# Optimization experiments

Hardware: AMD Instinct MI355X
Metric: run time of the kernel (lower is better)

## Reference

```python
import jax, jax.numpy as jnp
import numpy as np
import math

B, N, D = 16, 2048, 256

def setup_inputs() -> dict:
    key = jax.random.key(0)
    kq, kk, kv = jax.random.split(key, 3)
    query = jax.random.normal(kq, (B, N, D), dtype=jnp.float32)
    k = jax.random.normal(kk, (B, N, D), dtype=jnp.float32)
    value = jax.random.normal(kv, (B, D, N), dtype=jnp.float32)  # channel-first [B, d_v, N]
    return {"query": query, "key": k, "value": value, "mask": 0}

def reference(query, key, value, mask):
    d_k = query.shape[-1]
    scale = 1.0 / math.sqrt(d_k)
    # scores: [B, N, N]
    scores = jnp.einsum('bnd,bmd->bnm', query, key) * scale
    p_attn = jax.nn.softmax(scores, axis=-1)
    # mask is a static Python int flag gating dropout; mask=0 -> no dropout (deterministic reference)
    if mask:
        pass  # dropout intentionally disabled in deterministic reference
    # out = p_attn @ value^T  -> [B, N, d_v]; module returns out.transpose(-2,-1) -> [B, d_v, N]
    out_t = jnp.einsum('bnm,bdm->bdn', p_attn, value)
    return (out_t, p_attn)
```

## Files before the change

kernel.cpp:

```cpp
#include <hip/hip_runtime.h>
#include <hip/hip_bf16.h>


using bf16x8 = __attribute__((ext_vector_type(8))) short;
using f32x4  = __attribute__((ext_vector_type(4))) float;

__device__ __forceinline__ short f2bf(float f) {
    unsigned u = __float_as_uint(f);
    u += 0x7fffu + ((u >> 16) & 1u);
    return (short)(u >> 16);
}

__device__ __forceinline__ f32x4 mfma16(bf16x8 a, bf16x8 b, f32x4 c) {
    return __builtin_amdgcn_mfma_f32_16x16x32_bf16(a, b, c, 0, 0, 0);
}

#define AS1(p) ((const __attribute__((address_space(1))) void*)(p))
#define AS3(p) ((__attribute__((address_space(3))) void*)(p))

__global__ __launch_bounds__(256)
void convert_qkv(const float* __restrict__ Q, const float* __restrict__ K,
                 const float* __restrict__ V, short* __restrict__ Qb,
                 short* __restrict__ Kb, short* __restrict__ Vb, size_t n8)
{
    size_t i = (size_t)blockIdx.x * 256 + threadIdx.x;
    const float* src;
    short* dst;
    float scale = 1.0f;
    if (i < n8)            { src = Q;  dst = Qb; scale = 0.0625f; }
    else if (i < 2 * n8)   { i -= n8;      src = K; dst = Kb; }
    else                   { i -= 2 * n8;  src = V; dst = Vb; }
    const f32x4* s4 = (const f32x4*)src;
    f32x4 a = __builtin_nontemporal_load(s4 + i * 2);
    f32x4 b = __builtin_nontemporal_load(s4 + i * 2 + 1);
    bf16x8 v;
    v[0] = f2bf(a[0] * scale); v[1] = f2bf(a[1] * scale);
    v[2] = f2bf(a[2] * scale); v[3] = f2bf(a[3] * scale);
    v[4] = f2bf(b[0] * scale); v[5] = f2bf(b[1] * scale);
    v[6] = f2bf(b[2] * scale); v[7] = f2bf(b[3] * scale);
    *(bf16x8*)(dst + i * 8) = v;
}

__global__ __launch_bounds__(512, 2)
void fused_attn(const short* __restrict__ Qb, const short* __restrict__ Kb,
                const short* __restrict__ Vb, float* __restrict__ Pout,
                float* __restrict__ outT)
{
    __shared__ __align__(16) short Klds[2][64 * 256];
    __shared__ __align__(16) short Vlds[2][256 * 64];
    __shared__ __align__(16) short Plds[128 * 64];
    float* lpart = (float*)Plds;

    constexpr float LOG2E = 1.4426950408889634f;

    const unsigned g  = blockIdx.x;
    const unsigned wg = (g & 7) * 32 + (g >> 3);
    const int b  = (int)(wg >> 4);
    const int nb = (int)(wg & 15);

    const int tid  = threadIdx.x;
    const int lane = tid & 63;
    const int wave = tid >> 6;
    const int wn  = wave >> 1;
    const int wm  = wave & 1;
    const int l15 = lane & 15;
    const int l4  = lane >> 4;

    const short* Kbase = Kb + (size_t)b * (2048 * 256);
    const short* Vbase = Vb + (size_t)b * (256 * 2048);

    const short* Qp = Qb + ((size_t)b * 2048 + (size_t)nb * 128) * 256;
    bf16x8 qf[2][8];
#pragma unroll
    for (int mf = 0; mf < 2; mf++)
#pragma unroll
        for (int ks = 0; ks < 8; ks++)
            qf[mf][ks] = *(const bf16x8*)(
                Qp + (size_t)(wn * 32 + mf * 16 + l15) * 256 + ks * 32 + l4 * 8);

    auto stage_k = [&](int t, int buf) {
#pragma unroll
        for (int i = 0; i < 4; i++) {
            int ml = i * 16 + wave * 2 + (lane >> 5);
            int c  = lane & 31;
            int cs = (c & 24) | ((c ^ ml) & 7);
            __builtin_amdgcn_global_load_lds(
                AS1(Kbase + (size_t)(t * 64 + ml) * 256 + cs * 8),
                AS3(&Klds[buf][i * 4096 + wave * 512]), 16, 0, 0);
        }
    };
    auto stage_v = [&](int t, int buf) {
#pragma unroll
        for (int i = 0; i < 4; i++) {
            int d  = i * 64 + wave * 8 + (lane >> 3);
            int c  = lane & 7;
            int cs = c ^ (d & 7);
            __builtin_amdgcn_global_load_lds(
                AS1(Vbase + (size_t)d * 2048 + t * 64 + cs * 8),
                AS3(&Vlds[buf][i * 4096 + wave * 512]), 16, 0, 0);
        }
    };

    auto qkt = [&](int buf, f32x4 sacT[2][2]) {
#pragma unroll
        for (int ks = 0; ks < 8; ks++) {
            bf16x8 kf[2];
#pragma unroll
            for (int nf = 0; nf < 2; nf++) {
                int m  = wm * 32 + nf * 16 + l15;
                int ch = (ks * 4 + l4) ^ (m & 7);
                kf[nf] = *(const bf16x8*)((const char*)&Klds[buf][0] + m * 512 + ch * 16);
            }
#pragma unroll
            for (int mf = 0; mf < 2; mf++)
#pragma unroll
                for (int nf = 0; nf < 2; nf++)
                    sacT[mf][nf] = mfma16(kf[nf], qf[mf][ks], sacT[mf][nf]);
        }
    };

    float lacc[2] = {0.f, 0.f};
    stage_k(0, 0);
    for (int t = 0; t < 32; t++) {
        __syncthreads();
        if (t + 1 < 32) stage_k(t + 1, (t + 1) & 1);
        f32x4 sacT[2][2];
#pragma unroll
        for (int mf = 0; mf < 2; mf++)
#pragma unroll
            for (int nf = 0; nf < 2; nf++)
                sacT[mf][nf] = f32x4{0.f, 0.f, 0.f, 0.f};
        qkt(t & 1, sacT);
#pragma unroll
        for (int mf = 0; mf < 2; mf++)
#pragma unroll
            for (int nf = 0; nf < 2; nf++)
#pragma unroll
                for (int r = 0; r < 4; r++)
                    lacc[mf] += exp2f(sacT[mf][nf][r] * LOG2E);
    }
#pragma unroll
    for (int mf = 0; mf < 2; mf++) {
        lacc[mf] += __shfl_xor(lacc[mf], 16);
        lacc[mf] += __shfl_xor(lacc[mf], 32);
    }
    if (l4 == 0) {
        lpart[wave * 32 + 0 * 16 + l15] = lacc[0];
        lpart[wave * 32 + 1 * 16 + l15] = lacc[1];
    }
    __syncthreads();
    float rl[2];
#pragma unroll
    for (int mf = 0; mf < 2; mf++)
        rl[mf] = 1.0f / (lpart[(wn * 2 + 0) * 32 + mf * 16 + l15] +
                         lpart[(wn * 2 + 1) * 32 + mf * 16 + l15]);

    f32x4 oac[4][4];
#pragma unroll
    for (int i = 0; i < 4; i++)
#pragma unroll
        for (int j = 0; j < 4; j++)
            oac[i][j] = f32x4{0.f, 0.f, 0.f, 0.f};

    stage_k(0, 0);
    stage_v(0, 0);
    float* prow = Pout + ((size_t)b * 2048 + (size_t)nb * 128) * 2048;

    for (int t = 0; t < 32; t++) {
        __syncthreads();
        f32x4 sacT[2][2];
#pragma unroll
        for (int mf = 0; mf < 2; mf++)
#pragma unroll
            for (int nf = 0; nf < 2; nf++)
                sacT[mf][nf] = f32x4{0.f, 0.f, 0.f, 0.f};
        qkt(t & 1, sacT);

        f32x4 pv4[2][2];
#pragma unroll
        for (int mf = 0; mf < 2; mf++)
#pragma unroll
            for (int nf = 0; nf < 2; nf++) {
#pragma unroll
                for (int r = 0; r < 4; r++)
                    pv4[mf][nf][r] = exp2f(sacT[mf][nf][r] * LOG2E) * rl[mf];
                short4 ps;
                ps.x = f2bf(pv4[mf][nf][0]); ps.y = f2bf(pv4[mf][nf][1]);
                ps.z = f2bf(pv4[mf][nf][2]); ps.w = f2bf(pv4[mf][nf][3]);
                const int n  = wn * 32 + mf * 16 + l15;
                const int mb = wm * 32 + nf * 16 + l4 * 4;
                const int ch = (mb >> 3) ^ (n & 7);
                *(short4*)((char*)Plds + n * 128 + ch * 16 + (mb & 7) * 2) = ps;
            }
        __syncthreads();

        if (t + 1 < 32) {
            stage_k(t + 1, (t + 1) & 1);
            stage_v(t + 1, (t + 1) & 1);
        }

#pragma unroll
        for (int mf = 0; mf < 2; mf++)
#pragma unroll
            for (int nf = 0; nf < 2; nf++) {
                const int n  = wn * 32 + mf * 16 + l15;
                const int m  = t * 64 + wm * 32 + nf * 16 + l4 * 4;
                __builtin_nontemporal_store(pv4[mf][nf],
                    (f32x4*)(prow + (size_t)n * 2048 + m));
            }

        const char* vb_ = (const char*)&Vlds[t & 1][0];
#pragma unroll
        for (int ksl = 0; ksl < 2; ksl++) {
            bf16x8 vf[4], pf[4];
#pragma unroll
            for (int mf4 = 0; mf4 < 4; mf4++) {
                const int d  = wn * 64 + mf4 * 16 + l15;
                const int ch = (ksl * 4 + l4) ^ (d & 7);
                vf[mf4] = *(const bf16x8*)(vb_ + d * 128 + ch * 16);
            }
#pragma unroll
            for (int nf4 = 0; nf4 < 4; nf4++) {
                const int n  = wm * 64 + nf4 * 16 + l15;
                const int ch = (ksl * 4 + l4) ^ (n & 7);
                pf[nf4] = *(const bf16x8*)((const char*)Plds + n * 128 + ch * 16);
            }
#pragma unroll
            for (int mf4 = 0; mf4 < 4; mf4++)
#pragma unroll
                for (int nf4 = 0; nf4 < 4; nf4++)
                    oac[mf4][nf4] = mfma16(vf[mf4], pf[nf4], oac[mf4][nf4]);
        }
    }

    float* op = outT + (size_t)b * (256 * 2048) + (size_t)nb * 128;
#pragma unroll
    for (int mf4 = 0; mf4 < 4; mf4++)
#pragma unroll
        for (int nf4 = 0; nf4 < 4; nf4++)
#pragma unroll
            for (int r = 0; r < 4; r++) {
                int d = wn * 64 + mf4 * 16 + l4 * 4 + r;
                int n = wm * 64 + nf4 * 16 + l15;
                op[(size_t)d * 2048 + n] = oac[mf4][nf4][r];
            }
}

template<int BM, int BN, int BK>
__global__ __launch_bounds__(256)
void gemm_abt(const float* __restrict__ A, const float* __restrict__ B,
              float* __restrict__ C, int M, int N, int K,
              long strideA, long strideB, long strideC, float scale)
{
    const int b  = blockIdx.z;
    const int bm = blockIdx.y;
    const int bn = blockIdx.x;
    A += (size_t)b * strideA;
    B += (size_t)b * strideB;
    C += (size_t)b * strideC;

    constexpr int LDT = BK + 8;
    __shared__ __align__(16) short Alds[BM][LDT];
    __shared__ __align__(16) short Blds[BN][LDT];

    const int tid  = threadIdx.x;
    const int lane = tid & 63;
    const int wave = tid >> 6;
    const int wr   = wave >> 1;
    const int wc   = wave & 1;

    f32x4 acc[4][4];
#pragma unroll
    for (int m = 0; m < 4; m++)
#pragma unroll
        for (int n = 0; n < 4; n++)
            acc[m][n] = f32x4{0.f, 0.f, 0.f, 0.f};

    const float* Ab = A + (size_t)(bm * BM) * K;
    const float* Bb = B + (size_t)(bn * BN) * K;

    const int tr  = tid >> 4;
    const int tc4 = (tid & 15) << 2;

    for (int k0 = 0; k0 < K; k0 += BK) {
        __syncthreads();
#pragma unroll
        for (int r = tr; r < BM; r += 16) {
            const float4 v = *(const float4*)(Ab + (size_t)r * K + k0 + tc4);
            short4 s;
            s.x = f2bf(v.x); s.y = f2bf(v.y); s.z = f2bf(v.z); s.w = f2bf(v.w);
            *(short4*)&Alds[r][tc4] = s;
        }
#pragma unroll
        for (int r = tr; r < BN; r += 16) {
            const float4 v = *(const float4*)(Bb + (size_t)r * K + k0 + tc4);
            short4 s;
            s.x = f2bf(v.x); s.y = f2bf(v.y); s.z = f2bf(v.z); s.w = f2bf(v.w);
            *(short4*)&Blds[r][tc4] = s;
        }
        __syncthreads();

#pragma unroll
        for (int kk = 0; kk < BK; kk += 32) {
            const int ko = kk + ((lane >> 4) << 3);
            bf16x8 af[4], bfr[4];
#pragma unroll
            for (int m = 0; m < 4; m++)
                af[m] = *(const bf16x8*)&Alds[wr * 64 + m * 16 + (lane & 15)][ko];
#pragma unroll
            for (int n = 0; n < 4; n++)
                bfr[n] = *(const bf16x8*)&Blds[wc * 64 + n * 16 + (lane & 15)][ko];
#pragma unroll
            for (int m = 0; m < 4; m++)
#pragma unroll
                for (int n = 0; n < 4; n++)
                    acc[m][n] = __builtin_amdgcn_mfma_f32_16x16x32_bf16(
                        af[m], bfr[n], acc[m][n], 0, 0, 0);
        }
    }

    float* Cb = C + (size_t)(bm * BM) * N + (size_t)bn * BN;
    const int rbase = wr * 64 + ((lane >> 4) << 2);
    const int cbase = wc * 64 + (lane & 15);
#pragma unroll
    for (int m = 0; m < 4; m++)
#pragma unroll
        for (int n = 0; n < 4; n++)
#pragma unroll
            for (int r = 0; r < 4; r++)
                Cb[(size_t)(rbase + m * 16 + r) * N + cbase + n * 16] =
                    acc[m][n][r] * scale;
}

__global__ __launch_bounds__(256)
void softmax_rows(float* __restrict__ P)
{
    const size_t row = blockIdx.x;
    float* p = P + row * 2048;
    const int tid  = threadIdx.x;
    const int lane = tid & 63;
    const int wave = tid >> 6;

    float4 v0 = ((const float4*)p)[tid];
    float4 v1 = ((const float4*)p)[tid + 256];

    float m = fmaxf(fmaxf(fmaxf(v0.x, v0.y), fmaxf(v0.z, v0.w)),
                    fmaxf(fmaxf(v1.x, v1.y), fmaxf(v1.z, v1.w)));
#pragma unroll
    for (int off = 32; off; off >>= 1) m = fmaxf(m, __shfl_xor(m, off));

    __shared__ float sred[4];
    __shared__ float ssum[4];
    if (lane == 0) sred[wave] = m;
    __syncthreads();
    m = fmaxf(fmaxf(sred[0], sred[1]), fmaxf(sred[2], sred[3]));

    v0.x = expf(v0.x - m); v0.y = expf(v0.y - m);
    v0.z = expf(v0.z - m); v0.w = expf(v0.w - m);
    v1.x = expf(v1.x - m); v1.y = expf(v1.y - m);
    v1.z = expf(v1.z - m); v1.w = expf(v1.w - m);

    float s = (v0.x + v0.y + v0.z + v0.w) + (v1.x + v1.y + v1.z + v1.w);
#pragma unroll
    for (int off = 32; off; off >>= 1) s += __shfl_xor(s, off);
    if (lane == 0) ssum[wave] = s;
    __syncthreads();
    s = ssum[0] + ssum[1] + ssum[2] + ssum[3];

    const float r = 1.0f / s;
    v0.x *= r; v0.y *= r; v0.z *= r; v0.w *= r;
    v1.x *= r; v1.y *= r; v1.z *= r; v1.w *= r;

    ((float4*)p)[tid]       = v0;
    ((float4*)p)[tid + 256] = v1;
}

extern "C" void kernel_launch(void* const* d_in, const int* in_sizes, int n_in,
                              void* d_out, int out_size, void* d_ws, size_t ws_size,
                              hipStream_t stream)
{
    const float* Q  = (const float*)d_in[0];
    const float* Kk = (const float*)d_in[1];
    const float* V  = (const float*)d_in[2];

    float* outT = (float*)d_out;
    float* P    = outT + (size_t)16 * 256 * 2048;

    const size_t nQ = (size_t)16 * 2048 * 256;
    const long sQK = (long)2048 * 256;
    const long sP  = (long)2048 * 2048;
    const long sO  = (long)256 * 2048;

    const size_t needQKV = 3 * nQ * sizeof(short);

    if (ws_size >= needQKV) {
        short* Qb = (short*)d_ws;
        short* Kb = Qb + nQ;
        short* Vb = Kb + nQ;

        convert_qkv<<<dim3((unsigned)(3 * nQ / 8 / 256)), 256, 0, stream>>>(
            Q, Kk, V, Qb, Kb, Vb, nQ / 8);

        fused_attn<<<dim3(256), 512, 0, stream>>>(Qb, Kb, Vb, P, outT);
    } else {
        gemm_abt<128, 128, 64><<<dim3(16, 16, 16), 256, 0, stream>>>(
            Q, Kk, P, 2048, 2048, 256, sQK, sQK, sP, 0.0625f);
        softmax_rows<<<dim3(16 * 2048), 256, 0, stream>>>(P);
        gemm_abt<128, 128, 64><<<dim3(16, 2, 16), 256, 0, stream>>>(
            V, P, outT, 256, 2048, 2048, sO, sP, sO, 1.0f);
    }
}
```

Baseline: 185.1 us.

## Use 128-row K tiles in the row-sum pass and raise MFMA wave priority

The first (row-sum) pass now stages 128 K rows per step. It uses the whole K and V LDS arrays as its two buffers, which halves the loop trips and barriers for that pass. The prefetch of the first K and V tiles for the second pass is moved earlier, so it overlaps the row-sum reduction. s_setprio is raised around the MFMA sections so matrix work is favoured over the store and exp waves. The cost is more accumulator registers in the first pass, which could add register pressure at 2 blocks per CU.

```diff
diff --git a/kernel.cpp b/kernel.cpp
--- a/kernel.cpp
+++ b/kernel.cpp
@@ -10,13 +10,14 @@
     u += 0x7fffu + ((u >> 16) & 1u);
     return (short)(u >> 16);
 }
-
 __device__ __forceinline__ f32x4 mfma16(bf16x8 a, bf16x8 b, f32x4 c) {
     return __builtin_amdgcn_mfma_f32_16x16x32_bf16(a, b, c, 0, 0, 0);
 }
 
 #define AS1(p) ((const __attribute__((address_space(1))) void*)(p))
 #define AS3(p) ((__attribute__((address_space(3))) void*)(p))
+
+constexpr float LOG2E = 1.4426950408889634f;
 
 __global__ __launch_bounds__(256)
 void convert_qkv(const float* __restrict__ Q, const float* __restrict__ K,
@@ -51,8 +52,6 @@
     __shared__ __align__(16) short Plds[128 * 64];
     float* lpart = (float*)Plds;
 
-    constexpr float LOG2E = 1.4426950408889634f;
-
     const unsigned g  = blockIdx.x;
     const unsigned wg = (g & 7) * 32 + (g >> 3);
     const int b  = (int)(wg >> 4);
@@ -100,8 +99,21 @@
                 AS3(&Vlds[buf][i * 4096 + wave * 512]), 16, 0, 0);
         }
     };
+    auto stage_k128 = [&](int t, int which) {
+#pragma unroll
+        for (int i = 0; i < 8; i++) {
+            int ml = i * 16 + wave * 2 + (lane >> 5);
+            int c  = lane & 31;
+            int cs = (c & 24) | ((c ^ ml) & 7);
+            short* dst = which ? &Vlds[0][0] : &Klds[0][0];
+            __builtin_amdgcn_global_load_lds(
+                AS1(Kbase + (size_t)(t * 128 + ml) * 256 + cs * 8),
+                AS3(dst + i * 4096 + wave * 512), 16, 0, 0);
+        }
+    };
 
     auto qkt = [&](int buf, f32x4 sacT[2][2]) {
+        __builtin_amdgcn_s_setprio(1);
 #pragma unroll
         for (int ks = 0; ks < 8; ks++) {
             bf16x8 kf[2];
@@ -117,28 +129,50 @@
                 for (int nf = 0; nf < 2; nf++)
                     sacT[mf][nf] = mfma16(kf[nf], qf[mf][ks], sacT[mf][nf]);
         }
+        __builtin_amdgcn_s_setprio(0);
     };
+    auto qkt128 = [&](int which, f32x4 sacT[2][4]) {
+        const char* kb = which ? (const char*)&Vlds[0][0] : (const char*)&Klds[0][0];
+        __builtin_amdgcn_s_setprio(1);
+#pragma unroll
+        for (int ks = 0; ks < 8; ks++) {
+            bf16x8 kf[4];
+#pragma unroll
+            for (int nf = 0; nf < 4; nf++) {
+                int m  = wm * 64 + nf * 16 + l15;
+                int ch = (ks * 4 + l4) ^ (m & 7);
+                kf[nf] = *(const bf16x8*)(kb + m * 512 + ch * 16);
+            }
+#pragma unroll
+            for (int mf = 0; mf < 2; mf++)
+#pragma unroll
+                for (int nf = 0; nf < 4; nf++)
+                    sacT[mf][nf] = mfma16(kf[nf], qf[mf][ks], sacT[mf][nf]);
+        }
+        __builtin_amdgcn_s_setprio(0);
+    };
 
     float lacc[2] = {0.f, 0.f};
-    stage_k(0, 0);
-    for (int t = 0; t < 32; t++) {
+    stage_k128(0, 0);
+    for (int t = 0; t < 16; t++) {
         __syncthreads();
-        if (t + 1 < 32) stage_k(t + 1, (t + 1) & 1);
-        f32x4 sacT[2][2];
+        if (t + 1 < 16) stage_k128(t + 1, (t + 1) & 1);
+        f32x4 sacT[2][4];
 #pragma unroll
         for (int mf = 0; mf < 2; mf++)
 #pragma unroll
-            for (int nf = 0; nf < 2; nf++)
+            for (int nf = 0; nf < 4; nf++)
                 sacT[mf][nf] = f32x4{0.f, 0.f, 0.f, 0.f};
-        qkt(t & 1, sacT);
+        qkt128(t & 1, sacT);
 #pragma unroll
         for (int mf = 0; mf < 2; mf++)
 #pragma unroll
-            for (int nf = 0; nf < 2; nf++)
+            for (int nf = 0; nf < 4; nf++)
 #pragma unroll
                 for (int r = 0; r < 4; r++)
                     lacc[mf] += exp2f(sacT[mf][nf][r] * LOG2E);
     }
+    stage_k(0, 0);
 #pragma unroll
     for (int mf = 0; mf < 2; mf++) {
         lacc[mf] += __shfl_xor(lacc[mf], 16);
@@ -149,6 +183,7 @@
         lpart[wave * 32 + 1 * 16 + l15] = lacc[1];
     }
     __syncthreads();
+    stage_v(0, 0);
     float rl[2];
 #pragma unroll
     for (int mf = 0; mf < 2; mf++)
@@ -162,8 +197,6 @@
         for (int j = 0; j < 4; j++)
             oac[i][j] = f32x4{0.f, 0.f, 0.f, 0.f};
 
-    stage_k(0, 0);
-    stage_v(0, 0);
     float* prow = Pout + ((size_t)b * 2048 + (size_t)nb * 128) * 2048;
 
     for (int t = 0; t < 32; t++) {
@@ -210,6 +243,7 @@
             }
 
         const char* vb_ = (const char*)&Vlds[t & 1][0];
+        __builtin_amdgcn_s_setprio(1);
 #pragma unroll
         for (int ksl = 0; ksl < 2; ksl++) {
             bf16x8 vf[4], pf[4];
@@ -231,6 +265,7 @@
                 for (int nf4 = 0; nf4 < 4; nf4++)
                     oac[mf4][nf4] = mfma16(vf[mf4], pf[nf4], oac[mf4][nf4]);
         }
+        __builtin_amdgcn_s_setprio(0);
     }
 
     float* op = outT + (size_t)b * (256 * 2048) + (size_t)nb * 128;
```

Result: faster. 176.5 us (-4.6%).

## Deepen K prefetch ring and overlap staging with compute using partial-wait barriers

Applied to the files above, without the earlier changes.

In the first (row-sum) pass, the K and V shared-memory buffers are reused as a four-slot ring of K tiles, so each tile is prefetched two steps ahead. Custom barriers wait only on the older loads (vmcnt(4)) instead of draining all memory traffic. In the second pass, the K/V loads for the next tile are issued right after QK^T, and the fp32 P stores move ahead of the LDS P write. One full barrier per iteration is dropped, and MFMA sections are bracketed with s_setprio. The goal is to hide global-load latency and cut barrier stalls, but correctness now depends on hand-counted vmcnt values and on the order of async LDS loads versus stores.

```diff
diff --git a/kernel.cpp b/kernel.cpp
--- a/kernel.cpp
+++ b/kernel.cpp
@@ -10,13 +10,21 @@
     u += 0x7fffu + ((u >> 16) & 1u);
     return (short)(u >> 16);
 }
-
 __device__ __forceinline__ f32x4 mfma16(bf16x8 a, bf16x8 b, f32x4 c) {
     return __builtin_amdgcn_mfma_f32_16x16x32_bf16(a, b, c, 0, 0, 0);
 }
 
+__device__ __forceinline__ void bar_lgkm() {
+    asm volatile("s_waitcnt lgkmcnt(0)\n\ts_barrier" ::: "memory");
+}
+__device__ __forceinline__ void bar_vm4() {
+    asm volatile("s_waitcnt vmcnt(4) lgkmcnt(0)\n\ts_barrier" ::: "memory");
+}
+
 #define AS1(p) ((const __attribute__((address_space(1))) void*)(p))
 #define AS3(p) ((__attribute__((address_space(3))) void*)(p))
+
+constexpr float LOG2E = 1.4426950408889634f;
 
 __global__ __launch_bounds__(256)
 void convert_qkv(const float* __restrict__ Q, const float* __restrict__ K,
@@ -51,8 +59,6 @@
     __shared__ __align__(16) short Plds[128 * 64];
     float* lpart = (float*)Plds;
 
-    constexpr float LOG2E = 1.4426950408889634f;
-
     const unsigned g  = blockIdx.x;
     const unsigned wg = (g & 7) * 32 + (g >> 3);
     const int b  = (int)(wg >> 4);
@@ -100,8 +106,28 @@
                 AS3(&Vlds[buf][i * 4096 + wave * 512]), 16, 0, 0);
         }
     };
-
-    auto qkt = [&](int buf, f32x4 sacT[2][2]) {
+    auto stage64 = [&](int t, int bi) {
+        short* dst = (bi == 0) ? &Klds[0][0] : (bi == 1) ? &Klds[1][0]
+                   : (bi == 2) ? &Vlds[0][0] : &Vlds[1][0];
+#pragma unroll
+        for (int i = 0; i < 4; i++) {
+            int ml = i * 16 + wave * 2 + (lane >> 5);
+            int c  = lane & 31;
+            int cs = (c & 24) | ((c ^ ml) & 7);
+            __builtin_amdgcn_global_load_lds(
+                AS1(Kbase + (size_t)(t * 64 + ml) * 256 + cs * 8),
+                AS3(dst + i * 4096 + wave * 512), 16, 0, 0);
+        }
+    };
+    auto kb4 = [&](int i) -> const char* {
+        return (i == 0) ? (const char*)&Klds[0][0]
+             : (i == 1) ? (const char*)&Klds[1][0]
+             : (i == 2) ? (const char*)&Vlds[0][0]
+             :            (const char*)&Vlds[1][0];
+    };
+
+    auto qkt_p = [&](const char* kb, f32x4 sacT[2][2]) {
+        __builtin_amdgcn_s_setprio(1);
 #pragma unroll
         for (int ks = 0; ks < 8; ks++) {
             bf16x8 kf[2];
@@ -109,7 +135,7 @@
             for (int nf = 0; nf < 2; nf++) {
                 int m  = wm * 32 + nf * 16 + l15;
                 int ch = (ks * 4 + l4) ^ (m & 7);
-                kf[nf] = *(const bf16x8*)((const char*)&Klds[buf][0] + m * 512 + ch * 16);
+                kf[nf] = *(const bf16x8*)(kb + m * 512 + ch * 16);
             }
 #pragma unroll
             for (int mf = 0; mf < 2; mf++)
@@ -117,20 +143,23 @@
                 for (int nf = 0; nf < 2; nf++)
                     sacT[mf][nf] = mfma16(kf[nf], qf[mf][ks], sacT[mf][nf]);
         }
+        __builtin_amdgcn_s_setprio(0);
     };
 
     float lacc[2] = {0.f, 0.f};
-    stage_k(0, 0);
+    stage64(0, 0);
+    stage64(1, 1);
     for (int t = 0; t < 32; t++) {
-        __syncthreads();
-        if (t + 1 < 32) stage_k(t + 1, (t + 1) & 1);
+        if (t < 31) bar_vm4();
+        else        __syncthreads();
+        if (t + 2 < 32) stage64(t + 2, (t + 2) & 3);
         f32x4 sacT[2][2];
 #pragma unroll
         for (int mf = 0; mf < 2; mf++)
 #pragma unroll
             for (int nf = 0; nf < 2; nf++)
                 sacT[mf][nf] = f32x4{0.f, 0.f, 0.f, 0.f};
-        qkt(t & 1, sacT);
+        qkt_p(kb4(t & 3), sacT);
 #pragma unroll
         for (int mf = 0; mf < 2; mf++)
 #pragma unroll
@@ -139,6 +168,7 @@
                 for (int r = 0; r < 4; r++)
                     lacc[mf] += exp2f(sacT[mf][nf][r] * LOG2E);
     }
+    stage_k(0, 0);
 #pragma unroll
     for (int mf = 0; mf < 2; mf++) {
         lacc[mf] += __shfl_xor(lacc[mf], 16);
@@ -149,6 +179,7 @@
         lpart[wave * 32 + 1 * 16 + l15] = lacc[1];
     }
     __syncthreads();
+    stage_v(0, 0);
     float rl[2];
 #pragma unroll
     for (int mf = 0; mf < 2; mf++)
@@ -162,28 +193,46 @@
         for (int j = 0; j < 4; j++)
             oac[i][j] = f32x4{0.f, 0.f, 0.f, 0.f};
 
-    stage_k(0, 0);
-    stage_v(0, 0);
     float* prow = Pout + ((size_t)b * 2048 + (size_t)nb * 128) * 2048;
 
+    __syncthreads();
+
     for (int t = 0; t < 32; t++) {
-        __syncthreads();
         f32x4 sacT[2][2];
 #pragma unroll
         for (int mf = 0; mf < 2; mf++)
 #pragma unroll
             for (int nf = 0; nf < 2; nf++)
                 sacT[mf][nf] = f32x4{0.f, 0.f, 0.f, 0.f};
-        qkt(t & 1, sacT);
+        qkt_p((const char*)&Klds[t & 1][0], sacT);
+
+        if (t + 1 < 32) {
+            stage_k(t + 1, (t + 1) & 1);
+            stage_v(t + 1, (t + 1) & 1);
+        }
 
         f32x4 pv4[2][2];
 #pragma unroll
         for (int mf = 0; mf < 2; mf++)
 #pragma unroll
-            for (int nf = 0; nf < 2; nf++) {
+            for (int nf = 0; nf < 2; nf++)
 #pragma unroll
                 for (int r = 0; r < 4; r++)
                     pv4[mf][nf][r] = exp2f(sacT[mf][nf][r] * LOG2E) * rl[mf];
+#pragma unroll
+        for (int mf = 0; mf < 2; mf++)
+#pragma unroll
+            for (int nf = 0; nf < 2; nf++) {
+                const int n  = wn * 32 + mf * 16 + l15;
+                const int m  = t * 64 + wm * 32 + nf * 16 + l4 * 4;
+                __builtin_nontemporal_store(pv4[mf][nf],
+                    (f32x4*)(prow + (size_t)n * 2048 + m));
+            }
+
+#pragma unroll
+        for (int mf = 0; mf < 2; mf++)
+#pragma unroll
+            for (int nf = 0; nf < 2; nf++) {
                 short4 ps;
                 ps.x = f2bf(pv4[mf][nf][0]); ps.y = f2bf(pv4[mf][nf][1]);
                 ps.z = f2bf(pv4[mf][nf][2]); ps.w = f2bf(pv4[mf][nf][3]);
@@ -192,24 +241,10 @@
                 const int ch = (mb >> 3) ^ (n & 7);
                 *(short4*)((char*)Plds + n * 128 + ch * 16 + (mb & 7) * 2) = ps;
             }
-        __syncthreads();
-
-        if (t + 1 < 32) {
-            stage_k(t + 1, (t + 1) & 1);
-            stage_v(t + 1, (t + 1) & 1);
-        }
-
-#pragma unroll
-        for (int mf = 0; mf < 2; mf++)
-#pragma unroll
-            for (int nf = 0; nf < 2; nf++) {
-                const int n  = wn * 32 + mf * 16 + l15;
-                const int m  = t * 64 + wm * 32 + nf * 16 + l4 * 4;
-                __builtin_nontemporal_store(pv4[mf][nf],
-                    (f32x4*)(prow + (size_t)n * 2048 + m));
-            }
+        bar_lgkm();
 
         const char* vb_ = (const char*)&Vlds[t & 1][0];
+        __builtin_amdgcn_s_setprio(1);
 #pragma unroll
         for (int ksl = 0; ksl < 2; ksl++) {
             bf16x8 vf[4], pf[4];
@@ -231,6 +266,9 @@
                 for (int nf4 = 0; nf4 < 4; nf4++)
                     oac[mf4][nf4] = mfma16(vf[mf4], pf[nf4], oac[mf4][nf4]);
         }
+        __builtin_amdgcn_s_setprio(0);
+
+        bar_vm4();
     }
 
     float* op = outT + (size_t)b * (256 * 2048) + (size_t)nb * 128;
```

New measurement: 167.2 us. -9.7%, faster.
